# Optimization experiments

Hardware: AMD Instinct MI355X
Metric: run time of the kernel (lower is better)

The kernel has to match this reference:

```python
import jax, jax.numpy as jnp
import numpy as np

H = 32          # num_attention_heads
ROPE_BASE = 10000.0


def _rotary_freqs_cis(seq_len: int, head_dim: int) -> jnp.ndarray:
    # complex e^{i * pos * theta_j}, shape [seq_len, head_dim//2]
    inv_freq = 1.0 / (ROPE_BASE ** (jnp.arange(0, head_dim, 2, dtype=jnp.float32) / head_dim))
    angles = jnp.arange(seq_len, dtype=jnp.float32)[:, None] * inv_freq[None, :]
    return jax.lax.complex(jnp.cos(angles), jnp.sin(angles))


def _apply_rotary(u: jnp.ndarray, freqs_cis: jnp.ndarray) -> jnp.ndarray:
    # u: [B, S, H, hd]; faithful to apply_rotary_emb (interleaved pairs -> complex mul)
    ur = u.astype(jnp.float32).reshape(*u.shape[:-1], -1, 2)
    uc = jax.lax.complex(ur[..., 0], ur[..., 1])
    # freqs_cis broadcast: [1, S, 1, hd//2]
    uc = uc * freqs_cis[None, :, None, :]
    return jnp.stack((jnp.real(uc), jnp.imag(uc)), axis=-1).reshape(u.shape)


def setup_inputs() -> dict:
    key = jax.random.key(0)
    ks = jax.random.split(key, 5)
    B, S, D = 1, 2048, 4096
    init_std = 0.02
    x = jax.random.normal(ks[0], (B, S, D), dtype=jnp.float32)
    wq = jax.random.normal(ks[1], (D, D), dtype=jnp.float32) * init_std
    wk = jax.random.normal(ks[2], (D, D), dtype=jnp.float32) * init_std
    wv = jax.random.normal(ks[3], (D, D), dtype=jnp.float32) * init_std
    wo = jax.random.normal(ks[4], (D, D), dtype=jnp.float32) * init_std
    return {"x": x, "wq": wq, "wk": wk, "wv": wv, "wo": wo}


def reference(x, wq, wk, wv, wo):
    B, S, D = x.shape
    hd = D // H  # head_dim = 128
    q = (x @ wq).reshape(B, S, H, hd)
    k = (x @ wk).reshape(B, S, H, hd)
    v = (x @ wv).reshape(B, S, H, hd)

    freqs_cis = _rotary_freqs_cis(S, hd)
    q = _apply_rotary(q, freqs_cis)
    k = _apply_rotary(k, freqs_cis)
    # n_rep == 1 (num_key_value_heads == num_attention_heads) -> repeat_kv is identity

    scale = 1.0 / jnp.sqrt(jnp.float32(hd))
    scores = jnp.einsum('bqhd,bkhd->bhqk', q, k) * scale  # [B, H, S, S]
    causal = jnp.tril(jnp.ones((S, S), dtype=bool))
    neg = jnp.finfo(scores.dtype).min
    scores = jnp.where(causal[None, None, :, :], scores, neg)
    probs = jax.nn.softmax(scores, axis=-1)
    attn = jnp.einsum('bhqk,bkhd->bqhd', probs, v).reshape(B, S, D)
    return attn @ wo
```

## Files before the change

kernel.cpp:

```cpp
#include <hip/hip_runtime.h>
#include <stdint.h>

#define S_LEN 2048
#define DMODEL 4096
#define NHEAD 32
#define HDIM 128

typedef __attribute__((ext_vector_type(8))) short bf16x8;
typedef __attribute__((ext_vector_type(4))) float f32x4;

__device__ __forceinline__ unsigned short f2bf(float f) {
    union { float f; unsigned u; } v; v.f = f;
    unsigned u = v.u;
    unsigned r = (u + 0x7FFFu + ((u >> 16) & 1u)) >> 16;
    return (unsigned short)r;
}
__device__ __forceinline__ float bf2f(unsigned short h) {
    union { unsigned u; float f; } v; v.u = ((unsigned)h) << 16;
    return v.f;
}

__global__ void convert_x_kernel(const float* __restrict__ x,
                                 unsigned short* __restrict__ xb, int n4) {
    int t = blockIdx.x * blockDim.x + threadIdx.x;
    if (t >= n4) return;
    float4 v = ((const float4*)x)[t];
    ushort4 o;
    o.x = f2bf(v.x); o.y = f2bf(v.y); o.z = f2bf(v.z); o.w = f2bf(v.w);
    ((ushort4*)xb)[t] = o;
}

__global__ void convert_wt_kernel(const float* __restrict__ w,
                                  unsigned short* __restrict__ wt) {
    __shared__ unsigned short t[64][65];
    int n0 = blockIdx.x * 64, k0 = blockIdx.y * 64;
    for (int i = 0; i < 16; ++i) {
        int o = threadIdx.x + i * 256;
        int r = o >> 6, c = o & 63;
        t[r][c] = f2bf(w[(size_t)(k0 + r) * DMODEL + n0 + c]);
    }
    __syncthreads();
    for (int i = 0; i < 16; ++i) {
        int o = threadIdx.x + i * 256;
        int rr = o >> 6, kk = o & 63;
        wt[(size_t)(n0 + rr) * DMODEL + k0 + kk] = t[kk][rr];
    }
}


#define MFMA16(a, b, c) __builtin_amdgcn_mfma_f32_16x16x32_bf16(a, b, c, 0, 0, 0)

#define GLDS(g, l) __builtin_amdgcn_global_load_lds( \
    (__attribute__((address_space(1))) unsigned int*)(g), \
    (__attribute__((address_space(3))) unsigned int*)(l), 16, 0, 0)

#define VMCNT_(n) asm volatile("s_waitcnt vmcnt(" #n ")" ::: "memory")
#define VMCNT(n) VMCNT_(n)

#define PH_SYNC() \
    __builtin_amdgcn_sched_barrier(0); \
    __builtin_amdgcn_s_barrier(); \
    asm volatile("s_waitcnt lgkmcnt(0)" ::: "memory"); \
    __builtin_amdgcn_sched_barrier(0)

#define PH_END() \
    __builtin_amdgcn_s_setprio(0); \
    __builtin_amdgcn_sched_barrier(0); \
    __builtin_amdgcn_s_barrier(); \
    __builtin_amdgcn_sched_barrier(0)

#define PH_END_VM(VM) \
    __builtin_amdgcn_s_setprio(0); \
    __builtin_amdgcn_sched_barrier(0); \
    VMCNT(VM); \
    __builtin_amdgcn_s_barrier(); \
    __builtin_amdgcn_sched_barrier(0)

#define STAGE_A(T, PAR, J) do { \
    size_t ko_ = (size_t)(T) * 64 + (J) * 32; \
    GLDS(gA0 + ko_, As + ((PAR) * 2 + (J)) * 8192 + w * 512); \
    GLDS(gA1 + ko_, As + ((PAR) * 2 + (J)) * 8192 + 4096 + w * 512); \
} while (0)
#define STAGE_B(T, PAR, J) do { \
    size_t ko_ = (size_t)(T) * 64 + (J) * 32; \
    GLDS(gB + ko_, Bs + ((PAR) * 2 + (J)) * 4096 + w * 512); \
} while (0)

#define TILE(T, P, S1, S2, VM2, VM4) do { \
    const unsigned short* AsT = As + (P) * 16384; \
    const unsigned short* BsT = Bs + (P) * 8192; \
    bf16x8 af0, af1, af2, af3, bf0, bf1, bf2, bf3; \
     \
    af0 = *(const bf16x8*)&AsT[offA0]; \
    af1 = *(const bf16x8*)&AsT[offA1]; \
    af2 = *(const bf16x8*)&AsT[offA2]; \
    af3 = *(const bf16x8*)&AsT[offA3]; \
    bf0 = *(const bf16x8*)&BsT[offB0]; \
    bf1 = *(const bf16x8*)&BsT[offB1]; \
    if (S1) STAGE_A((T) + 1, (P) ^ 1, 1); \
    PH_SYNC(); \
    __builtin_amdgcn_s_setprio(1); \
    acc[0][0] = MFMA16(af0, bf0, acc[0][0]); \
    acc[1][0] = MFMA16(af1, bf0, acc[1][0]); \
    acc[2][0] = MFMA16(af2, bf0, acc[2][0]); \
    acc[3][0] = MFMA16(af3, bf0, acc[3][0]); \
    acc[0][1] = MFMA16(af0, bf1, acc[0][1]); \
    acc[1][1] = MFMA16(af1, bf1, acc[1][1]); \
    acc[2][1] = MFMA16(af2, bf1, acc[2][1]); \
    acc[3][1] = MFMA16(af3, bf1, acc[3][1]); \
    PH_END(); \
     \
    bf2 = *(const bf16x8*)&BsT[offB2]; \
    bf3 = *(const bf16x8*)&BsT[offB3]; \
    if (S1) STAGE_B((T) + 1, (P) ^ 1, 1); \
    PH_SYNC(); \
    __builtin_amdgcn_s_setprio(1); \
    acc[0][2] = MFMA16(af0, bf2, acc[0][2]); \
    acc[1][2] = MFMA16(af1, bf2, acc[1][2]); \
    acc[2][2] = MFMA16(af2, bf2, acc[2][2]); \
    acc[3][2] = MFMA16(af3, bf2, acc[3][2]); \
    acc[0][3] = MFMA16(af0, bf3, acc[0][3]); \
    acc[1][3] = MFMA16(af1, bf3, acc[1][3]); \
    acc[2][3] = MFMA16(af2, bf3, acc[2][3]); \
    acc[3][3] = MFMA16(af3, bf3, acc[3][3]); \
    PH_END_VM(VM2); \
     \
    af0 = *(const bf16x8*)&AsT[8192 + offA0]; \
    af1 = *(const bf16x8*)&AsT[8192 + offA1]; \
    af2 = *(const bf16x8*)&AsT[8192 + offA2]; \
    af3 = *(const bf16x8*)&AsT[8192 + offA3]; \
    bf0 = *(const bf16x8*)&BsT[4096 + offB0]; \
    bf1 = *(const bf16x8*)&BsT[4096 + offB1]; \
    if (S2) STAGE_A((T) + 2, (P), 0); \
    PH_SYNC(); \
    __builtin_amdgcn_s_setprio(1); \
    acc[0][0] = MFMA16(af0, bf0, acc[0][0]); \
    acc[1][0] = MFMA16(af1, bf0, acc[1][0]); \
    acc[2][0] = MFMA16(af2, bf0, acc[2][0]); \
    acc[3][0] = MFMA16(af3, bf0, acc[3][0]); \
    acc[0][1] = MFMA16(af0, bf1, acc[0][1]); \
    acc[1][1] = MFMA16(af1, bf1, acc[1][1]); \
    acc[2][1] = MFMA16(af2, bf1, acc[2][1]); \
    acc[3][1] = MFMA16(af3, bf1, acc[3][1]); \
    PH_END(); \
     \
    bf2 = *(const bf16x8*)&BsT[4096 + offB2]; \
    bf3 = *(const bf16x8*)&BsT[4096 + offB3]; \
    if (S2) STAGE_B((T) + 2, (P), 0); \
    PH_SYNC(); \
    __builtin_amdgcn_s_setprio(1); \
    acc[0][2] = MFMA16(af0, bf2, acc[0][2]); \
    acc[1][2] = MFMA16(af1, bf2, acc[1][2]); \
    acc[2][2] = MFMA16(af2, bf2, acc[2][2]); \
    acc[3][2] = MFMA16(af3, bf2, acc[3][2]); \
    acc[0][3] = MFMA16(af0, bf3, acc[0][3]); \
    acc[1][3] = MFMA16(af1, bf3, acc[1][3]); \
    acc[2][3] = MFMA16(af2, bf3, acc[2][3]); \
    acc[3][3] = MFMA16(af3, bf3, acc[3][3]); \
    PH_END_VM(VM4); \
} while (0)

template<int STORE_MODE>
__global__ __launch_bounds__(512, 2)
void gemm8p_kernel(const unsigned short* __restrict__ A,
                   const unsigned short* __restrict__ BT,
                   void* __restrict__ C) {
    constexpr int M = S_LEN, N = DMODEL, K = DMODEL;
    constexpr int NT = K / 64;
    extern __shared__ __align__(16) unsigned short sm[];
    unsigned short* As = sm;
    unsigned short* Bs = sm + 32768;

    const int tid = threadIdx.x;
    const int lane = tid & 63;
    const int w = tid >> 6;
    const int wr = w >> 1, wc = w & 1;
    const int q = lane >> 4, lm = lane & 15;

    int orig = blockIdx.y * gridDim.x + blockIdx.x;
    const int by = orig & 7;
    const int bx = orig >> 3;
    const int m0 = by * 256, n0 = bx * 128;

    const int c4 = tid & 3, r4 = tid >> 2, s4 = (tid >> 3) & 3;
    const unsigned short* gA0 = A + (size_t)(m0 + r4) * K + ((c4 ^ s4) * 8);
    const unsigned short* gA1 = gA0 + (size_t)128 * K;
    const unsigned short* gB  = BT + (size_t)(n0 + r4) * K + ((c4 ^ s4) * 8);

#define FRAGOFF(r_) ((r_) * 32 + ((q ^ (((r_) >> 1) & 3)) * 8))
    const int rA = wr * 64 + lm, rB = wc * 64 + lm;
    const int offA0 = FRAGOFF(rA);
    const int offA1 = FRAGOFF(rA + 16);
    const int offA2 = FRAGOFF(rA + 32);
    const int offA3 = FRAGOFF(rA + 48);
    const int offB0 = FRAGOFF(rB);
    const int offB1 = FRAGOFF(rB + 16);
    const int offB2 = FRAGOFF(rB + 32);
    const int offB3 = FRAGOFF(rB + 48);
#undef FRAGOFF

    f32x4 zero = {0.f, 0.f, 0.f, 0.f};
    f32x4 acc[4][4];
    for (int i = 0; i < 4; ++i)
        for (int j = 0; j < 4; ++j) acc[i][j] = zero;

    STAGE_A(0, 0, 0); STAGE_B(0, 0, 0);
    STAGE_A(0, 0, 1); STAGE_B(0, 0, 1);
    STAGE_A(1, 1, 0); STAGE_B(1, 1, 0);
    VMCNT(6);
    __builtin_amdgcn_s_barrier();
    __builtin_amdgcn_sched_barrier(0);

    for (int t = 0; t < NT - 2; t += 2) {
        TILE(t, 0, true, true, 6, 6);
        TILE(t + 1, 1, true, true, 6, 6);
    }
    TILE(NT - 2, 0, true, false, 6, 3);
    TILE(NT - 1, 1, false, false, 0, 0);

    for (int mi = 0; mi < 4; ++mi) {
        int mbase = m0 + wr * 64 + mi * 16 + q * 4;
        for (int ni = 0; ni < 4; ++ni) {
            int n = n0 + wc * 64 + ni * 16 + lm;
            if (STORE_MODE == 0) {
                unsigned short* Cb = (unsigned short*)C;
                for (int r = 0; r < 4; ++r)
                    Cb[(size_t)(mbase + r) * N + n] = f2bf(acc[mi][ni][r]);
            } else if (STORE_MODE == 1) {
                unsigned short* Cb = (unsigned short*)C;
                ushort4 v;
                v.x = f2bf(acc[mi][ni][0]); v.y = f2bf(acc[mi][ni][1]);
                v.z = f2bf(acc[mi][ni][2]); v.w = f2bf(acc[mi][ni][3]);
                *(ushort4*)&Cb[(size_t)n * M + mbase] = v;
            } else {
                float* Cf = (float*)C;
                for (int r = 0; r < 4; ++r)
                    Cf[(size_t)(mbase + r) * N + n] = acc[mi][ni][r];
            }
        }
    }
}

__global__ void rope_kernel(unsigned short* __restrict__ qb,
                            unsigned short* __restrict__ kb) {
    int t = blockIdx.x * blockDim.x + threadIdx.x;
    if (t >= S_LEN * DMODEL / 2) return;
    int s = t >> 11;
    int p = t & 2047;
    int j = p & 63;
    float ang = (float)s * exp2f((float)j * -0.2076205059304602f);
    float sn, cs;
    sincosf(ang, &sn, &cs);
    size_t idx = (size_t)s * DMODEL + 2 * p;
    const float SC = 0.08838834764831845f;
    float a0 = bf2f(qb[idx]), a1 = bf2f(qb[idx + 1]);
    qb[idx]     = f2bf((a0 * cs - a1 * sn) * SC);
    qb[idx + 1] = f2bf((a0 * sn + a1 * cs) * SC);
    float b0 = bf2f(kb[idx]), b1 = bf2f(kb[idx + 1]);
    kb[idx]     = f2bf(b0 * cs - b1 * sn);
    kb[idx + 1] = f2bf(b0 * sn + b1 * cs);
}

__global__ __launch_bounds__(256, 2)
void attn_kernel(const unsigned short* __restrict__ qb,
                 const unsigned short* __restrict__ kb,
                 const unsigned short* __restrict__ vt,
                 unsigned short* __restrict__ ab) {
    __shared__ __align__(16) unsigned short Ks[64 * 128];
    __shared__ __align__(16) unsigned short VTs[128 * 64];
    __shared__ __align__(16) unsigned short Pb[4][16 * 72];
    const int t = threadIdx.x;
    const int lane = t & 63;
    const int w = t >> 6;
    const int h = blockIdx.y;
    const int q0 = ((int)gridDim.x - 1 - (int)blockIdx.x) * 64;
    const int qw = q0 + w * 16;
    const int q = lane >> 4, lm = lane & 15;

    const int krow = t >> 2;
    const int kcol = t & 3;
    const int vrow = t >> 1;
    const int vcol = t & 1;

    const unsigned short* gK = kb + (size_t)krow * DMODEL + h * HDIM;
    const unsigned short* gV = vt + (size_t)(h * HDIM + vrow) * S_LEN;

    bf16x8 qf[4];
    for (int kc = 0; kc < 4; ++kc)
        qf[kc] = *(const bf16x8*)&qb[(size_t)(qw + lm) * DMODEL + h * HDIM + kc * 32 + q * 8];

    f32x4 zero = {0.f, 0.f, 0.f, 0.f};
    f32x4 o[8];
    for (int i = 0; i < 8; ++i) o[i] = zero;
    float mrow[4] = {-1e30f, -1e30f, -1e30f, -1e30f};
    float lrow[4] = {0.f, 0.f, 0.f, 0.f};

    const int nch = q0 / 64 + 1;

    bf16x8 kreg[4], vreg[4];
    for (int i = 0; i < 4; ++i) {
        kreg[i] = *(const bf16x8*)&gK[(size_t)0 * DMODEL + (kcol + i * 4) * 8];
        vreg[i] = *(const bf16x8*)&gV[0 + (vcol + i * 2) * 8];
    }
    for (int i = 0; i < 4; ++i) {
        *(bf16x8*)&Ks[krow * 128 + (((kcol + i * 4) ^ (krow & 15)) * 8)] = kreg[i];
        *(bf16x8*)&VTs[vrow * 64 + (((vcol + i * 2) ^ (vrow & 7)) * 8)] = vreg[i];
    }
    __syncthreads();

    for (int c = 0; c < nch; ++c) {
        const int j0 = c * 64;
        if (c + 1 < nch) {
            const size_t jn = (size_t)(j0 + 64);
            for (int i = 0; i < 4; ++i) {
                kreg[i] = *(const bf16x8*)&gK[jn * DMODEL + (kcol + i * 4) * 8];
                vreg[i] = *(const bf16x8*)&gV[jn + (vcol + i * 2) * 8];
            }
        }

        f32x4 s[4];
        for (int ks = 0; ks < 4; ++ks) s[ks] = zero;
        for (int kc = 0; kc < 4; ++kc)
            for (int ks = 0; ks < 4; ++ks) {
                bf16x8 kf = *(const bf16x8*)&Ks[(ks * 16 + lm) * 128 + (((kc * 4 + q) ^ lm) * 8)];
                s[ks] = __builtin_amdgcn_mfma_f32_16x16x32_bf16(qf[kc], kf, s[ks], 0, 0, 0);
            }
        if (c == nch - 1) {
            for (int ks = 0; ks < 4; ++ks)
                for (int r = 0; r < 4; ++r)
                    if (j0 + ks * 16 + lm > qw + q * 4 + r) s[ks][r] = -1e30f;
        }
        float al[4];
        for (int r = 0; r < 4; ++r) {
            float mx = fmaxf(fmaxf(s[0][r], s[1][r]), fmaxf(s[2][r], s[3][r]));
            mx = fmaxf(mx, __shfl_xor(mx, 1));
            mx = fmaxf(mx, __shfl_xor(mx, 2));
            mx = fmaxf(mx, __shfl_xor(mx, 4));
            mx = fmaxf(mx, __shfl_xor(mx, 8));
            float mn = fmaxf(mrow[r], mx);
            al[r] = __expf(mrow[r] - mn);
            mrow[r] = mn;
            float rs = 0.f;
            float pv[4];
            for (int ks = 0; ks < 4; ++ks) {
                pv[ks] = __expf(s[ks][r] - mn);
                rs += pv[ks];
            }
            rs += __shfl_xor(rs, 1);
            rs += __shfl_xor(rs, 2);
            rs += __shfl_xor(rs, 4);
            rs += __shfl_xor(rs, 8);
            lrow[r] = lrow[r] * al[r] + rs;
            for (int ks = 0; ks < 4; ++ks)
                Pb[w][(q * 4 + r) * 72 + ks * 16 + lm] = f2bf(pv[ks]);
        }
        bf16x8 pA0 = *(const bf16x8*)&Pb[w][lm * 72 + q * 8];
        bf16x8 pA1 = *(const bf16x8*)&Pb[w][lm * 72 + 32 + q * 8];
        for (int nt = 0; nt < 8; ++nt) {
            int d = nt * 16 + lm;
            bf16x8 vf0 = *(const bf16x8*)&VTs[d * 64 + ((q ^ (d & 7)) * 8)];
            bf16x8 vf1 = *(const bf16x8*)&VTs[d * 64 + (((4 + q) ^ (d & 7)) * 8)];
            f32x4 oo = o[nt];
            for (int r = 0; r < 4; ++r) oo[r] *= al[r];
            oo = __builtin_amdgcn_mfma_f32_16x16x32_bf16(pA0, vf0, oo, 0, 0, 0);
            o[nt] = __builtin_amdgcn_mfma_f32_16x16x32_bf16(pA1, vf1, oo, 0, 0, 0);
        }

        __syncthreads();
        if (c + 1 < nch) {
            for (int i = 0; i < 4; ++i) {
                *(bf16x8*)&Ks[krow * 128 + (((kcol + i * 4) ^ (krow & 15)) * 8)] = kreg[i];
                *(bf16x8*)&VTs[vrow * 64 + (((vcol + i * 2) ^ (vrow & 7)) * 8)] = vreg[i];
            }
        }
        __syncthreads();
    }

    float inv[4];
    for (int r = 0; r < 4; ++r) inv[r] = 1.0f / lrow[r];
    for (int nt = 0; nt < 8; ++nt) {
        int d = h * HDIM + lm + nt * 16;
        for (int r = 0; r < 4; ++r)
            ab[(size_t)(qw + q * 4 + r) * DMODEL + d] = f2bf(o[nt][r] * inv[r]);
    }
}

extern "C" void kernel_launch(void* const* d_in, const int* in_sizes, int n_in,
                              void* d_out, int out_size, void* d_ws, size_t ws_size,
                              hipStream_t stream) {
    const float* x  = (const float*)d_in[0];
    const float* wq = (const float*)d_in[1];
    const float* wk = (const float*)d_in[2];
    const float* wv = (const float*)d_in[3];
    const float* wo = (const float*)d_in[4];
    char* ws = (char*)d_ws;
    const size_t MB = 1024 * 1024;
    unsigned short* xb  = (unsigned short*)(ws + 0 * MB);
    unsigned short* qb  = (unsigned short*)(ws + 16 * MB);
    unsigned short* kb  = (unsigned short*)(ws + 32 * MB);
    unsigned short* vtb = (unsigned short*)(ws + 48 * MB);
    unsigned short* ab  = (unsigned short*)(ws + 64 * MB);
    unsigned short* wtb = (unsigned short*)(ws + 80 * MB);

    static int attr_done = 0;
    if (!attr_done) {
        hipFuncSetAttribute((const void*)&gemm8p_kernel<0>,
                            hipFuncAttributeMaxDynamicSharedMemorySize, 98304);
        hipFuncSetAttribute((const void*)&gemm8p_kernel<1>,
                            hipFuncAttributeMaxDynamicSharedMemorySize, 98304);
        hipFuncSetAttribute((const void*)&gemm8p_kernel<2>,
                            hipFuncAttributeMaxDynamicSharedMemorySize, 98304);
        attr_done = 1;
    }

    dim3 cg(64, 64);
    dim3 gg(32, 8);

    convert_x_kernel<<<(S_LEN * DMODEL / 4) / 256, 256, 0, stream>>>(x, xb, S_LEN * DMODEL / 4);

    convert_wt_kernel<<<cg, 256, 0, stream>>>(wq, wtb);
    gemm8p_kernel<0><<<gg, 512, 98304, stream>>>(xb, wtb, qb);
    convert_wt_kernel<<<cg, 256, 0, stream>>>(wk, wtb);
    gemm8p_kernel<0><<<gg, 512, 98304, stream>>>(xb, wtb, kb);
    convert_wt_kernel<<<cg, 256, 0, stream>>>(wv, wtb);
    gemm8p_kernel<1><<<gg, 512, 98304, stream>>>(xb, wtb, vtb);

    rope_kernel<<<(S_LEN * DMODEL / 2) / 256, 256, 0, stream>>>(qb, kb);

    attn_kernel<<<dim3(S_LEN / 64, NHEAD), 256, 0, stream>>>(qb, kb, vtb, ab);

    convert_wt_kernel<<<cg, 256, 0, stream>>>(wo, wtb);
    gemm8p_kernel<2><<<gg, 512, 98304, stream>>>(ab, wtb, d_out);
}
```

Before: 728.0 us.

## Process 128 queries per attention block with two 16-row tiles per wave

The attention kernel now handles 128 query rows per block, with 32 per wave split into two 16-row MFMA tiles. Each K/V chunk loaded into shared memory is reused across twice as many queries, halving the global K/V traffic and the number of staging syncs per query. Waves skip chunks that lie entirely above their causal diagonal. In exchange the kernel uses more registers (two sets of output accumulators and softmax state), launches half as many blocks, and lets waves within a block diverge in work near the diagonal.

New measurement: 721.9 us. No clear change (-0.8%).

```diff
diff --git a/kernel.cpp b/kernel.cpp
--- a/kernel.cpp
+++ b/kernel.cpp
@@ -90,7 +90,6 @@
     const unsigned short* AsT = As + (P) * 16384; \
     const unsigned short* BsT = Bs + (P) * 8192; \
     bf16x8 af0, af1, af2, af3, bf0, bf1, bf2, bf3; \
-     \
     af0 = *(const bf16x8*)&AsT[offA0]; \
     af1 = *(const bf16x8*)&AsT[offA1]; \
     af2 = *(const bf16x8*)&AsT[offA2]; \
@@ -109,7 +108,6 @@
     acc[2][1] = MFMA16(af2, bf1, acc[2][1]); \
     acc[3][1] = MFMA16(af3, bf1, acc[3][1]); \
     PH_END(); \
-     \
     bf2 = *(const bf16x8*)&BsT[offB2]; \
     bf3 = *(const bf16x8*)&BsT[offB3]; \
     if (S1) STAGE_B((T) + 1, (P) ^ 1, 1); \
@@ -124,7 +122,6 @@
     acc[2][3] = MFMA16(af2, bf3, acc[2][3]); \
     acc[3][3] = MFMA16(af3, bf3, acc[3][3]); \
     PH_END_VM(VM2); \
-     \
     af0 = *(const bf16x8*)&AsT[8192 + offA0]; \
     af1 = *(const bf16x8*)&AsT[8192 + offA1]; \
     af2 = *(const bf16x8*)&AsT[8192 + offA2]; \
@@ -143,7 +140,6 @@
     acc[2][1] = MFMA16(af2, bf1, acc[2][1]); \
     acc[3][1] = MFMA16(af3, bf1, acc[3][1]); \
     PH_END(); \
-     \
     bf2 = *(const bf16x8*)&BsT[4096 + offB2]; \
     bf3 = *(const bf16x8*)&BsT[4096 + offB3]; \
     if (S2) STAGE_B((T) + 2, (P), 0); \
@@ -268,13 +264,13 @@
                  unsigned short* __restrict__ ab) {
     __shared__ __align__(16) unsigned short Ks[64 * 128];
     __shared__ __align__(16) unsigned short VTs[128 * 64];
-    __shared__ __align__(16) unsigned short Pb[4][16 * 72];
+    __shared__ __align__(16) unsigned short Pb[4][32 * 72];
     const int t = threadIdx.x;
     const int lane = t & 63;
     const int w = t >> 6;
     const int h = blockIdx.y;
-    const int q0 = ((int)gridDim.x - 1 - (int)blockIdx.x) * 64;
-    const int qw = q0 + w * 16;
+    const int q0 = ((int)gridDim.x - 1 - (int)blockIdx.x) * 128;
+    const int qw = q0 + w * 32;
     const int q = lane >> 4, lm = lane & 15;
 
     const int krow = t >> 2;
@@ -285,23 +281,33 @@
     const unsigned short* gK = kb + (size_t)krow * DMODEL + h * HDIM;
     const unsigned short* gV = vt + (size_t)(h * HDIM + vrow) * S_LEN;
 
-    bf16x8 qf[4];
-    for (int kc = 0; kc < 4; ++kc)
-        qf[kc] = *(const bf16x8*)&qb[(size_t)(qw + lm) * DMODEL + h * HDIM + kc * 32 + q * 8];
+    bf16x8 qf[2][4];
+#pragma unroll
+    for (int qt = 0; qt < 2; ++qt)
+#pragma unroll
+        for (int kc = 0; kc < 4; ++kc)
+            qf[qt][kc] = *(const bf16x8*)&qb[(size_t)(qw + qt * 16 + lm) * DMODEL
+                                            + h * HDIM + kc * 32 + q * 8];
 
     f32x4 zero = {0.f, 0.f, 0.f, 0.f};
-    f32x4 o[8];
-    for (int i = 0; i < 8; ++i) o[i] = zero;
-    float mrow[4] = {-1e30f, -1e30f, -1e30f, -1e30f};
-    float lrow[4] = {0.f, 0.f, 0.f, 0.f};
-
-    const int nch = q0 / 64 + 1;
+    f32x4 o[2][8];
+#pragma unroll
+    for (int qt = 0; qt < 2; ++qt)
+        for (int i = 0; i < 8; ++i) o[qt][i] = zero;
+    float mrow[2][4], lrow[2][4];
+#pragma unroll
+    for (int qt = 0; qt < 2; ++qt)
+        for (int r = 0; r < 4; ++r) { mrow[qt][r] = -1e30f; lrow[qt][r] = 0.f; }
+
+    const int nch = q0 / 64 + 2;
 
     bf16x8 kreg[4], vreg[4];
+#pragma unroll
     for (int i = 0; i < 4; ++i) {
         kreg[i] = *(const bf16x8*)&gK[(size_t)0 * DMODEL + (kcol + i * 4) * 8];
         vreg[i] = *(const bf16x8*)&gV[0 + (vcol + i * 2) * 8];
     }
+#pragma unroll
     for (int i = 0; i < 4; ++i) {
         *(bf16x8*)&Ks[krow * 128 + (((kcol + i * 4) ^ (krow & 15)) * 8)] = kreg[i];
         *(bf16x8*)&VTs[vrow * 64 + (((vcol + i * 2) ^ (vrow & 7)) * 8)] = vreg[i];
@@ -312,62 +318,120 @@
         const int j0 = c * 64;
         if (c + 1 < nch) {
             const size_t jn = (size_t)(j0 + 64);
+#pragma unroll
             for (int i = 0; i < 4; ++i) {
                 kreg[i] = *(const bf16x8*)&gK[jn * DMODEL + (kcol + i * 4) * 8];
                 vreg[i] = *(const bf16x8*)&gV[jn + (vcol + i * 2) * 8];
             }
         }
 
-        f32x4 s[4];
-        for (int ks = 0; ks < 4; ++ks) s[ks] = zero;
-        for (int kc = 0; kc < 4; ++kc)
-            for (int ks = 0; ks < 4; ++ks) {
-                bf16x8 kf = *(const bf16x8*)&Ks[(ks * 16 + lm) * 128 + (((kc * 4 + q) ^ lm) * 8)];
-                s[ks] = __builtin_amdgcn_mfma_f32_16x16x32_bf16(qf[kc], kf, s[ks], 0, 0, 0);
+        if (j0 <= qw + 31) {
+            f32x4 s[2][4];
+#pragma unroll
+            for (int qt = 0; qt < 2; ++qt)
+                for (int ks = 0; ks < 4; ++ks) s[qt][ks] = zero;
+#pragma unroll
+            for (int kc = 0; kc < 4; ++kc)
+#pragma unroll
+                for (int ks = 0; ks < 4; ++ks) {
+                    bf16x8 kf = *(const bf16x8*)&Ks[(ks * 16 + lm) * 128
+                                                    + (((kc * 4 + q) ^ lm) * 8)];
+                    s[0][ks] = __builtin_amdgcn_mfma_f32_16x16x32_bf16(qf[0][kc], kf, s[0][ks], 0, 0, 0);
+                    s[1][ks] = __builtin_amdgcn_mfma_f32_16x16x32_bf16(qf[1][kc], kf, s[1][ks], 0, 0, 0);
+                }
+            if (j0 + 63 > qw) {
+#pragma unroll
+                for (int qt = 0; qt < 2; ++qt)
+#pragma unroll
+                    for (int ks = 0; ks < 4; ++ks)
+#pragma unroll
+                        for (int r = 0; r < 4; ++r)
+                            if (j0 + ks * 16 + lm > qw + qt * 16 + q * 4 + r)
+                                s[qt][ks][r] = -1e30f;
             }
-        if (c == nch - 1) {
-            for (int ks = 0; ks < 4; ++ks)
+
+            float mx[2][4];
+#pragma unroll
+            for (int qt = 0; qt < 2; ++qt)
+#pragma unroll
                 for (int r = 0; r < 4; ++r)
-                    if (j0 + ks * 16 + lm > qw + q * 4 + r) s[ks][r] = -1e30f;
-        }
-        float al[4];
-        for (int r = 0; r < 4; ++r) {
-            float mx = fmaxf(fmaxf(s[0][r], s[1][r]), fmaxf(s[2][r], s[3][r]));
-            mx = fmaxf(mx, __shfl_xor(mx, 1));
-            mx = fmaxf(mx, __shfl_xor(mx, 2));
-            mx = fmaxf(mx, __shfl_xor(mx, 4));
-            mx = fmaxf(mx, __shfl_xor(mx, 8));
-            float mn = fmaxf(mrow[r], mx);
-            al[r] = __expf(mrow[r] - mn);
-            mrow[r] = mn;
-            float rs = 0.f;
-            float pv[4];
-            for (int ks = 0; ks < 4; ++ks) {
-                pv[ks] = __expf(s[ks][r] - mn);
-                rs += pv[ks];
+                    mx[qt][r] = fmaxf(fmaxf(s[qt][0][r], s[qt][1][r]),
+                                      fmaxf(s[qt][2][r], s[qt][3][r]));
+#pragma unroll
+            for (int st = 1; st <= 8; st <<= 1)
+#pragma unroll
+                for (int qt = 0; qt < 2; ++qt)
+#pragma unroll
+                    for (int r = 0; r < 4; ++r)
+                        mx[qt][r] = fmaxf(mx[qt][r], __shfl_xor(mx[qt][r], st));
+
+            float aln[2][4], mnv[2][4], rs[2][4];
+#pragma unroll
+            for (int qt = 0; qt < 2; ++qt)
+#pragma unroll
+                for (int r = 0; r < 4; ++r) {
+                    mnv[qt][r] = fmaxf(mrow[qt][r], mx[qt][r]);
+                    aln[qt][r] = __expf(mrow[qt][r] - mnv[qt][r]);
+                    mrow[qt][r] = mnv[qt][r];
+                }
+#pragma unroll
+            for (int qt = 0; qt < 2; ++qt)
+#pragma unroll
+                for (int ks = 0; ks < 4; ++ks)
+#pragma unroll
+                    for (int r = 0; r < 4; ++r)
+                        s[qt][ks][r] = __expf(s[qt][ks][r] - mnv[qt][r]);
+#pragma unroll
+            for (int qt = 0; qt < 2; ++qt)
+#pragma unroll
+                for (int r = 0; r < 4; ++r)
+                    rs[qt][r] = (s[qt][0][r] + s[qt][1][r]) + (s[qt][2][r] + s[qt][3][r]);
+#pragma unroll
+            for (int st = 1; st <= 8; st <<= 1)
+#pragma unroll
+                for (int qt = 0; qt < 2; ++qt)
+#pragma unroll
+                    for (int r = 0; r < 4; ++r)
+                        rs[qt][r] += __shfl_xor(rs[qt][r], st);
+#pragma unroll
+            for (int qt = 0; qt < 2; ++qt)
+#pragma unroll
+                for (int r = 0; r < 4; ++r)
+                    lrow[qt][r] = lrow[qt][r] * aln[qt][r] + rs[qt][r];
+
+#pragma unroll
+            for (int qt = 0; qt < 2; ++qt)
+#pragma unroll
+                for (int ks = 0; ks < 4; ++ks)
+#pragma unroll
+                    for (int r = 0; r < 4; ++r)
+                        Pb[w][(qt * 16 + q * 4 + r) * 72 + ks * 16 + lm] = f2bf(s[qt][ks][r]);
+
+            bf16x8 pA[2][2];
+#pragma unroll
+            for (int qt = 0; qt < 2; ++qt) {
+                pA[qt][0] = *(const bf16x8*)&Pb[w][(qt * 16 + lm) * 72 + q * 8];
+                pA[qt][1] = *(const bf16x8*)&Pb[w][(qt * 16 + lm) * 72 + 32 + q * 8];
             }
-            rs += __shfl_xor(rs, 1);
-            rs += __shfl_xor(rs, 2);
-            rs += __shfl_xor(rs, 4);
-            rs += __shfl_xor(rs, 8);
-            lrow[r] = lrow[r] * al[r] + rs;
-            for (int ks = 0; ks < 4; ++ks)
-                Pb[w][(q * 4 + r) * 72 + ks * 16 + lm] = f2bf(pv[ks]);
-        }
-        bf16x8 pA0 = *(const bf16x8*)&Pb[w][lm * 72 + q * 8];
-        bf16x8 pA1 = *(const bf16x8*)&Pb[w][lm * 72 + 32 + q * 8];
-        for (int nt = 0; nt < 8; ++nt) {
-            int d = nt * 16 + lm;
-            bf16x8 vf0 = *(const bf16x8*)&VTs[d * 64 + ((q ^ (d & 7)) * 8)];
-            bf16x8 vf1 = *(const bf16x8*)&VTs[d * 64 + (((4 + q) ^ (d & 7)) * 8)];
-            f32x4 oo = o[nt];
-            for (int r = 0; r < 4; ++r) oo[r] *= al[r];
-            oo = __builtin_amdgcn_mfma_f32_16x16x32_bf16(pA0, vf0, oo, 0, 0, 0);
-            o[nt] = __builtin_amdgcn_mfma_f32_16x16x32_bf16(pA1, vf1, oo, 0, 0, 0);
+#pragma unroll
+            for (int nt = 0; nt < 8; ++nt) {
+                int d = nt * 16 + lm;
+                bf16x8 vf0 = *(const bf16x8*)&VTs[d * 64 + ((q ^ (d & 7)) * 8)];
+                bf16x8 vf1 = *(const bf16x8*)&VTs[d * 64 + (((4 + q) ^ (d & 7)) * 8)];
+#pragma unroll
+                for (int qt = 0; qt < 2; ++qt) {
+                    f32x4 oo = o[qt][nt];
+#pragma unroll
+                    for (int r = 0; r < 4; ++r) oo[r] *= aln[qt][r];
+                    oo = __builtin_amdgcn_mfma_f32_16x16x32_bf16(pA[qt][0], vf0, oo, 0, 0, 0);
+                    o[qt][nt] = __builtin_amdgcn_mfma_f32_16x16x32_bf16(pA[qt][1], vf1, oo, 0, 0, 0);
+                }
+            }
         }
 
         __syncthreads();
         if (c + 1 < nch) {
+#pragma unroll
             for (int i = 0; i < 4; ++i) {
                 *(bf16x8*)&Ks[krow * 128 + (((kcol + i * 4) ^ (krow & 15)) * 8)] = kreg[i];
                 *(bf16x8*)&VTs[vrow * 64 + (((vcol + i * 2) ^ (vrow & 7)) * 8)] = vreg[i];
@@ -376,13 +440,21 @@
         __syncthreads();
     }
 
-    float inv[4];
-    for (int r = 0; r < 4; ++r) inv[r] = 1.0f / lrow[r];
-    for (int nt = 0; nt < 8; ++nt) {
-        int d = h * HDIM + lm + nt * 16;
-        for (int r = 0; r < 4; ++r)
-            ab[(size_t)(qw + q * 4 + r) * DMODEL + d] = f2bf(o[nt][r] * inv[r]);
-    }
+    float inv[2][4];
+#pragma unroll
+    for (int qt = 0; qt < 2; ++qt)
+#pragma unroll
+        for (int r = 0; r < 4; ++r) inv[qt][r] = 1.0f / lrow[qt][r];
+#pragma unroll
+    for (int qt = 0; qt < 2; ++qt)
+#pragma unroll
+        for (int nt = 0; nt < 8; ++nt) {
+            int d = h * HDIM + lm + nt * 16;
+#pragma unroll
+            for (int r = 0; r < 4; ++r)
+                ab[(size_t)(qw + qt * 16 + q * 4 + r) * DMODEL + d] =
+                    f2bf(o[qt][nt][r] * inv[qt][r]);
+        }
 }
 
 extern "C" void kernel_launch(void* const* d_in, const int* in_sizes, int n_in,
@@ -427,7 +499,7 @@
 
     rope_kernel<<<(S_LEN * DMODEL / 2) / 256, 256, 0, stream>>>(qb, kb);
 
-    attn_kernel<<<dim3(S_LEN / 64, NHEAD), 256, 0, stream>>>(qb, kb, vtb, ab);
+    attn_kernel<<<dim3(S_LEN / 128, NHEAD), 256, 0, stream>>>(qb, kb, vtb, ab);
 
     convert_wt_kernel<<<cg, 256, 0, stream>>>(wo, wtb);
     gemm8p_kernel<2><<<gg, 512, 98304, stream>>>(ab, wtb, d_out);
```
